# Kernel optimization log

Hardware: AMD Instinct MI355X
Metric: run time of the kernel (lower is better)

The kernel has to match this reference:

```python
import jax, jax.numpy as jnp
import numpy as np

MAX_SEQ = 4096
HEADS = 4
LOCAL_HEADS = 1
WINDOW = 128
B, N, D_IN, D, D_OUT = 8, 3000, 128, 512, 64


def setup_inputs():
    key = jax.random.key(0)
    ks = jax.random.split(key, 9)
    s = 0.02
    return {
        'x': jax.random.normal(ks[0], (B, N, D_IN), jnp.float32),
        'W1': jax.random.normal(ks[1], (D_IN, D), jnp.float32) * s,
        'b1': jnp.zeros((D,), jnp.float32),
        'ln1_g': jnp.ones((D,), jnp.float32),
        'ln1_b': jnp.zeros((D,), jnp.float32),
        'Wq': jax.random.normal(ks[2], (D, D), jnp.float32) * s,
        'Wk': jax.random.normal(ks[3], (D, D), jnp.float32) * s,
        'Wv': jax.random.normal(ks[4], (D, D), jnp.float32) * s,
        'Wo': jax.random.normal(ks[5], (D, D), jnp.float32) * s,
        'bo': jnp.zeros((D,), jnp.float32),
        'ln2_g': jnp.ones((D,), jnp.float32),
        'ln2_b': jnp.zeros((D,), jnp.float32),
        'Wf1': jax.random.normal(ks[6], (D, 4 * D), jnp.float32) * s,
        'bf1': jnp.zeros((4 * D,), jnp.float32),
        'Wf2': jax.random.normal(ks[7], (4 * D, D), jnp.float32) * s,
        'bf2': jnp.zeros((D,), jnp.float32),
        'W2': jax.random.normal(ks[8], (D, D_OUT), jnp.float32) * s,
        'b2': jnp.zeros((D_OUT,), jnp.float32),
    }


def _ln(x, g, b, eps=1e-5):
    mu = jnp.mean(x, -1, keepdims=True)
    var = jnp.var(x, -1, keepdims=True)
    return (x - mu) * jax.lax.rsqrt(var + eps) * g + b


def _look_around(x, pad_value=0.0):
    # x: [b, w, n, ...] -> [b, w, 3n, ...] (backward=1, self, forward=1 windows)
    pads = [(0, 0), (1, 1)] + [(0, 0)] * (x.ndim - 2)
    p = jnp.pad(x, pads, constant_values=pad_value)
    w = x.shape[1]
    return jnp.concatenate([p[:, i:i + w] for i in range(3)], axis=2)


def _local_attn(q, k, v):
    # windowed softmax attention, window=128, look back/forward 1 window
    Bh, H, T, d = q.shape
    w = T // WINDOW
    merge = lambda t: t.reshape(Bh * H, w, WINDOW, d)
    bq, bk, bv = merge(q), merge(k), merge(v)
    bk = _look_around(bk)
    bv = _look_around(bv)
    ticker = jnp.arange(T).reshape(1, w, WINDOW)
    bq_k = _look_around(ticker, pad_value=-1)  # [1, w, 3*WINDOW]
    dots = jnp.einsum('bwie,bwje->bwij', bq, bk) * (d ** -0.5)
    mask = (bq_k[:, :, None, :] == -1)
    dots = jnp.where(mask, jnp.finfo(dots.dtype).min, dots)
    attn = jax.nn.softmax(dots, axis=-1)
    out = jnp.einsum('bwij,bwje->bwie', attn, bv)
    return out.reshape(Bh, H, T, d)


def _linear_attn(q, k, v):
    # kernelized global attention: softmax feature maps + d x d context
    d = q.shape[-1]
    q = jax.nn.softmax(q, axis=-1) * (d ** -0.5)
    k = jax.nn.softmax(k, axis=-2)
    ctx = jnp.einsum('bhnd,bhne->bhde', k, v)
    return jnp.einsum('bhnd,bhde->bhne', q, ctx)


def _self_attn(x, Wq, Wk, Wv, Wo, bo):
    Bx, T, Dm = x.shape
    dh = Dm // HEADS
    split = lambda t: t.reshape(Bx, T, HEADS, dh).transpose(0, 2, 1, 3)
    q, k, v = split(x @ Wq), split(x @ Wk), split(x @ Wv)
    lq, gq = q[:, :LOCAL_HEADS], q[:, LOCAL_HEADS:]
    lk, gk = k[:, :LOCAL_HEADS], k[:, LOCAL_HEADS:]
    lv, gv = v[:, :LOCAL_HEADS], v[:, LOCAL_HEADS:]
    local_out = _local_attn(lq, lk, lv)
    global_out = _linear_attn(gq, gk, gv)
    out = jnp.concatenate([local_out, global_out], axis=1)
    out = out.transpose(0, 2, 1, 3).reshape(Bx, T, Dm)
    return out @ Wo + bo


def _forward(x, W1, b1, ln1_g, ln1_b, Wq, Wk, Wv, Wo, bo,
             ln2_g, ln2_b, Wf1, bf1, Wf2, bf2, W2, b2):
    Bx, n, _ = x.shape
    xp = jnp.pad(x, ((0, 0), (0, MAX_SEQ - n), (0, 0)))
    h = jnp.tanh(xp @ W1 + b1)
    # depth=1 transformer block: PreNorm attn + residual, PreNorm FF + residual
    h = h + _self_attn(_ln(h, ln1_g, ln1_b), Wq, Wk, Wv, Wo, bo)
    ff = jax.nn.gelu(_ln(h, ln2_g, ln2_b) @ Wf1 + bf1, approximate=False)
    h = h + ff @ Wf2 + bf2
    out = h @ W2 + b2
    return out[:, :n, :]


def reference(x, W1, b1, ln1_g, ln1_b, Wq, Wk, Wv, Wo, bo,
              ln2_g, ln2_b, Wf1, bf1, Wf2, bf2, W2, b2):
    return _forward(x, W1, b1, ln1_g, ln1_b, Wq, Wk, Wv, Wo, bo,
                    ln2_g, ln2_b, Wf1, bf1, Wf2, bf2, W2, b2)
```

## Files before the change

### kernel.cpp

```cpp
#include <hip/hip_runtime.h>
#include <hip/hip_bf16.h>
#include <math.h>


typedef __hip_bfloat16 bf16;
typedef __attribute__((ext_vector_type(8))) short short8;
typedef __attribute__((ext_vector_type(4))) float floatx4;

#define SEQ   4096
#define NBAT  8
#define DM    512
#define DINP  128
#define DFF   2048
#define NREAL 3000
#define CS    40

#define MFMA16(a,b,c) __builtin_amdgcn_mfma_f32_16x16x32_bf16((a),(b),(c),0,0,0)
#define BARRIER() asm volatile("s_barrier" ::: "memory")

__device__ __forceinline__ void gload_lds16(const void* g, void* l) {
  auto* gp = reinterpret_cast<const __attribute__((address_space(1))) unsigned int*>(
      reinterpret_cast<uintptr_t>(g));
  auto* lp = reinterpret_cast<__attribute__((address_space(3))) unsigned int*>(
      reinterpret_cast<uintptr_t>(l));
  __builtin_amdgcn_global_load_lds(gp, lp, 16, 0, 0);
}

__device__ __forceinline__ short8 lds_read128(const bf16* p) {
  auto* lp = reinterpret_cast<const __attribute__((address_space(3))) bf16*>(
      reinterpret_cast<uintptr_t>(p));
  short8 r;
  asm volatile("ds_read_b128 %0, %1" : "=v"(r) : "v"(lp));
  return r;
}

__device__ __forceinline__ float fast_erff(float x) {
  float ax = fabsf(x);
  float t = __builtin_amdgcn_rcpf(fmaf(0.3275911f, ax, 1.f));
  float p = fmaf(fmaf(fmaf(fmaf(1.061405429f, t, -1.453152027f), t,
                           1.421413741f), t, -0.284496736f), t, 0.254829592f) * t;
  float r = 1.f - p * __expf(-ax * ax);
  return copysignf(r, x);
}

__device__ __forceinline__ float fast_tanhf(float x) {
  float e = __expf(2.f * x);
  return 1.f - 2.f * __builtin_amdgcn_rcpf(e + 1.f);
}

__global__ __launch_bounds__(256) void beacon(float* __restrict__ out, long n) {
  long i = (long)blockIdx.x * 256 + threadIdx.x;
  if (i < n) out[i] = 10000.f;
}

__global__ __launch_bounds__(256) void transpose8(
    const float* __restrict__ W1, const float* __restrict__ Wq,
    const float* __restrict__ Wk, const float* __restrict__ Wv,
    const float* __restrict__ Wo, const float* __restrict__ Wf1,
    const float* __restrict__ Wf2, const float* __restrict__ W2,
    bf16* __restrict__ wt) {
  const int Ks[8]   = {128, 512, 512, 512, 512, 512, 2048, 512};
  const int Ns[8]   = {512, 512, 512, 512, 512, 2048, 512, 64};
  const int Nps[8]  = {512, 512, 512, 512, 512, 2048, 512, 128};
  const long Ofs[8] = {0L, 65536L, 327680L, 589824L, 851968L, 1114112L, 2162688L, 3211264L};
  int zi = blockIdx.z;
  int K = Ks[zi], N = Ns[zi], Npad = Nps[zi];
  int k0 = blockIdx.x * 64, n0 = blockIdx.y * 64;
  if (k0 >= K || n0 >= Npad) return;
  const float* W = zi == 0 ? W1 : zi == 1 ? Wq : zi == 2 ? Wk : zi == 3 ? Wv
                 : zi == 4 ? Wo : zi == 5 ? Wf1 : zi == 6 ? Wf2 : W2;
  bf16* Wt = wt + Ofs[zi];
  __shared__ float t[64][65];
  int r = threadIdx.x >> 2, c = (threadIdx.x & 3) * 16;
#pragma unroll
  for (int i = 0; i < 16; i++) {
    int n = n0 + c + i;
    t[r][c + i] = (n < N) ? W[(long)(k0 + r) * N + n] : 0.f;
  }
  __syncthreads();
#pragma unroll
  for (int i = 0; i < 16; i++)
    Wt[(long)(n0 + r) * K + k0 + c + i] = (bf16)t[c + i][r];
}

__device__ inline uint4 pack8(const float* p) {
  union { bf16 h[8]; uint4 u; } r;
  float4 a = *(const float4*)p;
  float4 b = *(const float4*)(p + 4);
  r.h[0] = (bf16)a.x; r.h[1] = (bf16)a.y; r.h[2] = (bf16)a.z; r.h[3] = (bf16)a.w;
  r.h[4] = (bf16)b.x; r.h[5] = (bf16)b.y; r.h[6] = (bf16)b.z; r.h[7] = (bf16)b.w;
  return r.u;
}

__global__ __launch_bounds__(512, 2) void gemm256(
    const bf16* __restrict__ A, const bf16* __restrict__ Bt,
    const float* __restrict__ bias, float* __restrict__ Cf, bf16* __restrict__ Cb,
    int K, int lda, int ldb, int ldc, int EPI,
    long aBatch, long bBatch, int zdiv, long cOuter, long cInner) {
  __shared__ __align__(16) bf16 sm[2][2][256 * 64];
  const int tid = threadIdx.x;
  const int lane = tid & 63, wid = tid >> 6;

  const int nx = gridDim.x, ny = gridDim.y;
  const long nwg = (long)nx * ny * gridDim.z;
  const long fid = blockIdx.x + (long)nx * (blockIdx.y + (long)ny * blockIdx.z);
  const long cq = nwg >> 3, cr = nwg & 7;
  const long xcd = fid & 7, ofs = fid >> 3;
  const long swz = (xcd < cr ? xcd * (cq + 1) : cr * (cq + 1) + (xcd - cr) * cq) + ofs;
  const int bx = (int)(swz % nx);
  const int by = (int)((swz / nx) % ny);
  const int bz = (int)(swz / ((long)nx * ny));

  const bf16* Ab = A + (long)bz * aBatch;
  const bf16* Bb = Bt + (long)bz * bBatch;
  const long cOff = (long)(bz / zdiv) * cOuter + (long)(bz % zdiv) * cInner;
  const int row0 = by * 256;
  const int col0 = bx * 256;

  const int widm = wid >> 2, widn = wid & 3;
  const int lr = lane & 15, lq4 = lane >> 4;
  const int sw = (lr & 7) << 4;
  const int k0e = ((0 * 64 + lq4 * 16) ^ sw) >> 1;
  const int k1e = ((1 * 64 + lq4 * 16) ^ sw) >> 1;

  const int lrow = lane >> 3;
  const int lch = (lane & 7) ^ lrow;
  const bf16* pAbase = Ab + (long)(row0 + wid * 8 + lrow) * lda + lch * 8;
  const bf16* pBbase = Bb + (long)(col0 + wid * 8 + lrow) * ldb + lch * 8;
  const long a64 = (long)64 * lda, b64 = (long)64 * ldb;
  int kA = 0, kB = 0;

  floatx4 acc[8][4];
#pragma unroll
  for (int i = 0; i < 8; i++)
#pragma unroll
    for (int j = 0; j < 4; j++) acc[i][j] = {0.f, 0.f, 0.f, 0.f};

  auto stageA = [&](int buf, int h) {
    bf16* d = &sm[buf][0][(h * 128 + wid * 8) * 64];
    const bf16* g = pAbase + (long)(h * 2) * a64 + kA;
    gload_lds16(g, d);
    gload_lds16(g + a64, d + 64 * 64);
  };
  auto stageB = [&](int buf, int h) {
    bf16* d = &sm[buf][1][(h * 128 + wid * 8) * 64];
    const bf16* g = pBbase + (long)(h * 2) * b64 + kB;
    gload_lds16(g, d);
    gload_lds16(g + b64, d + 64 * 64);
  };

  short8 bfr[4][2], af[2][2];
  auto readB = [&](int buf) {
    const bf16* base = &sm[buf][1][0];
#pragma unroll
    for (int nt = 0; nt < 4; nt++) {
      int colB = widn * 64 + nt * 16 + lr;
      bfr[nt][0] = lds_read128(base + colB * 64 + k0e);
      bfr[nt][1] = lds_read128(base + colB * 64 + k1e);
    }
  };
  auto readA = [&](int buf, int q) {
    const bf16* base = &sm[buf][0][0];
#pragma unroll
    for (int m = 0; m < 2; m++) {
      int rowA = widm * 128 + q * 32 + m * 16 + lr;
      af[m][0] = lds_read128(base + rowA * 64 + k0e);
      af[m][1] = lds_read128(base + rowA * 64 + k1e);
    }
  };
  auto mmaq = [&](int q) {
    asm volatile("s_waitcnt lgkmcnt(0)" ::: "memory");
    __builtin_amdgcn_sched_barrier(0);
    __builtin_amdgcn_s_setprio(1);
#pragma unroll
    for (int m = 0; m < 2; m++)
#pragma unroll
      for (int nt = 0; nt < 4; nt++) {
        acc[q * 2 + m][nt] = MFMA16(af[m][0], bfr[nt][0], acc[q * 2 + m][nt]);
        acc[q * 2 + m][nt] = MFMA16(af[m][1], bfr[nt][1], acc[q * 2 + m][nt]);
      }
    __builtin_amdgcn_s_setprio(0);
  };

  const int T = K >> 6;
  stageA(0, 0); stageA(0, 1); kA += 64;
  stageB(0, 0); stageB(0, 1); kB += 64;
  stageB(1, 0); stageB(1, 1); kB += 64;
  asm volatile("s_waitcnt vmcnt(4)" ::: "memory");
  BARRIER();

  for (int t = 0; t < T; t++) {
    const int cb = t & 1, nb = cb ^ 1;
    readB(cb);
    readA(cb, 0);
    if (t + 1 < T) stageA(nb, 0);
    mmaq(0);
    BARRIER();
    readA(cb, 1);
    if (t + 1 < T) { stageA(nb, 1); kA += 64; }
    if (t + 2 < T) stageB(cb, 0);
    mmaq(1);
    BARRIER();
    readA(cb, 2);
    if (t + 2 < T) { stageB(cb, 1); kB += 64; }
    mmaq(2);
    BARRIER();
    readA(cb, 3);
    mmaq(3);
    if (t + 2 < T) {
      asm volatile("s_waitcnt vmcnt(4)" ::: "memory");
    } else if (t + 1 < T) {
      asm volatile("s_waitcnt vmcnt(0)" ::: "memory");
    }
    BARRIER();
  }

  if (EPI == 2) {
#pragma unroll
    for (int nt = 0; nt < 4; nt++) {
      int c = col0 + widn * 64 + nt * 16 + lr;
      float bv = bias ? bias[c] : 0.f;
#pragma unroll
      for (int mi = 0; mi < 8; mi++) {
        long rb = row0 + widm * 128 + mi * 16 + lq4 * 4;
#pragma unroll
        for (int reg = 0; reg < 4; reg++) {
          float v = acc[mi][nt][reg] + bv;
          long idx = cOff + (rb + reg) * (long)ldc + c;
          Cf[idx] += v;
        }
      }
    }
  } else {
    bf16* scr = ((bf16*)&sm[0][0][0]) + wid * (64 * 80);
    const int rr = lane >> 3, ccol = (lane & 7) * 8;
#pragma unroll
    for (int p = 0; p < 2; p++) {
#pragma unroll
      for (int nt = 0; nt < 4; nt++) {
        int c = col0 + widn * 64 + nt * 16 + lr;
        float bv = bias ? bias[c] : 0.f;
#pragma unroll
        for (int ml = 0; ml < 4; ml++) {
#pragma unroll
          for (int reg = 0; reg < 4; reg++) {
            float v = acc[p * 4 + ml][nt][reg] + bv;
            if (EPI == 4) v = 0.5f * v * (1.f + fast_erff(v * 0.70710678118654752f));
            scr[(ml * 16 + lq4 * 4 + reg) * 80 + nt * 16 + lr] = (bf16)v;
          }
        }
      }
#pragma unroll
      for (int it = 0; it < 8; it++) {
        int r = it * 8 + rr;
        uint4 v = *(const uint4*)&scr[r * 80 + ccol];
        long grow = row0 + widm * 128 + p * 64 + r;
        *(uint4*)&Cb[cOff + grow * (long)ldc + col0 + widn * 64 + ccol] = v;
      }
    }
  }
}

__global__ __launch_bounds__(256) void gemm_bt(
    const void* __restrict__ Avoid, const bf16* __restrict__ Bt,
    const float* __restrict__ bias, float* __restrict__ Cf, bf16* __restrict__ Cb,
    int K, int lda, int ldb, int ldc, int EPI, int AMODE,
    long aBatch, long bBatch, int zdiv, long cOuter, long cInner) {
  __shared__ __align__(16) bf16 As0[128 * 32];
  __shared__ __align__(16) bf16 As1[128 * 32];
  __shared__ __align__(16) bf16 Bs0[128 * 32];
  __shared__ __align__(16) bf16 Bs1[128 * 32];
  const int tid = threadIdx.x;

  const int nx = gridDim.x, ny = gridDim.y;
  const long nwg = (long)nx * ny * gridDim.z;
  const long fid = blockIdx.x + (long)nx * (blockIdx.y + (long)ny * blockIdx.z);
  const long cq = nwg >> 3, cr = nwg & 7;
  const long xcd = fid & 7, ofs = fid >> 3;
  const long swz = (xcd < cr ? xcd * (cq + 1) : cr * (cq + 1) + (xcd - cr) * cq) + ofs;
  const int bx = (int)(swz % nx);
  const int by = (int)((swz / nx) % ny);
  const int bz = (int)(swz / ((long)nx * ny));

  Bt += (long)bz * bBatch;
  const long cOff = (long)(bz / zdiv) * cOuter + (long)(bz % zdiv) * cInner;
  const int row0 = by * 128;
  const int col0 = bx * 128;
  const int lane = tid & 63, wid = tid >> 6;
  const int wm = (wid & 1) * 64, wn = (wid >> 1) * 64;
  const int lr = lane & 15, lk = (lane >> 4) * 8;

  floatx4 acc[4][4];
#pragma unroll
  for (int i = 0; i < 4; i++)
#pragma unroll
    for (int j = 0; j < 4; j++) acc[i][j] = {0.f, 0.f, 0.f, 0.f};

  if (AMODE == 0) {
    const bf16* A = (const bf16*)Avoid + (long)bz * aBatch;
    const bf16* pAa = A + (long)(row0 + wid * 16 + (lane >> 2)) * lda + (lane & 3) * 8;
    const bf16* pBa = Bt + (long)(col0 + wid * 16 + (lane >> 2)) * ldb + (lane & 3) * 8;
    bf16* ldsA0 = &As0[wid * 16 * 32];
    bf16* ldsA1 = &As1[wid * 16 * 32];
    bf16* ldsB0 = &Bs0[wid * 16 * 32];
    bf16* ldsB1 = &Bs1[wid * 16 * 32];
    const long a64 = (long)64 * lda, b64 = (long)64 * ldb;

    auto stage = [&](bf16* dA, bf16* dB) {
      gload_lds16(pAa, dA);
      gload_lds16(pAa + a64, dA + 64 * 32);
      gload_lds16(pBa, dB);
      gload_lds16(pBa + b64, dB + 64 * 32);
      pAa += 32; pBa += 32;
    };
    auto compute = [&](const bf16* AS, const bf16* BS) {
      short8 af[4], bfr[4];
#pragma unroll
      for (int mt = 0; mt < 4; mt++) af[mt] = *(const short8*)(&AS[(wm + mt * 16 + lr) * 32 + lk]);
#pragma unroll
      for (int nt = 0; nt < 4; nt++) bfr[nt] = *(const short8*)(&BS[(wn + nt * 16 + lr) * 32 + lk]);
#pragma unroll
      for (int mt = 0; mt < 4; mt++)
#pragma unroll
        for (int nt = 0; nt < 4; nt++)
          acc[mt][nt] = MFMA16(af[mt], bfr[nt], acc[mt][nt]);
    };

    stage(ldsA0, ldsB0);
    __syncthreads();
    for (int k0 = 0; k0 < K; k0 += 64) {
      stage(ldsA1, ldsB1);
      compute(As0, Bs0);
      __syncthreads();
      if (k0 + 64 < K) stage(ldsA0, ldsB0);
      compute(As1, Bs1);
      __syncthreads();
    }
  } else {
    const float* Af = (const float*)Avoid;
    const int srow = tid >> 2;
    const int skcol = (tid & 3) * 8;
    const long r0 = row0 + srow, r1 = r0 + 64;
    const bf16* pB = Bt + (long)(col0 + srow) * ldb + skcol;
    const int ldsOff = srow * 32 + skcol;
    const float* pF0; const float* pF1;
    bool v0 = true, v1 = true;
    if (AMODE == 1) {
      int t0 = (int)(r0 & (SEQ - 1)), t1 = (int)(r1 & (SEQ - 1));
      v0 = t0 < NREAL; v1 = t1 < NREAL;
      if (!v0) t0 = 0;
      if (!v1) t1 = 0;
      pF0 = Af + ((r0 >> 12) * NREAL + t0) * DINP + skcol;
      pF1 = Af + ((r1 >> 12) * NREAL + t1) * DINP + skcol;
    } else {
      pF0 = Af + r0 * lda + skcol;
      pF1 = Af + r1 * lda + skcol;
    }
    for (int k0 = 0; k0 < K; k0 += 32) {
      uint4 b0 = *(const uint4*)(pB);
      uint4 b1 = *(const uint4*)(pB + (long)64 * ldb);
      pB += 32;
      uint4 a0 = {0, 0, 0, 0}, a1 = {0, 0, 0, 0};
      if (v0) a0 = pack8(pF0);
      if (v1) a1 = pack8(pF1);
      pF0 += 32; pF1 += 32;
      __syncthreads();
      *(uint4*)(&As0[ldsOff]) = a0;
      *(uint4*)(&As0[ldsOff + 64 * 32]) = a1;
      *(uint4*)(&Bs0[ldsOff]) = b0;
      *(uint4*)(&Bs0[ldsOff + 64 * 32]) = b1;
      __syncthreads();
      short8 af[4], bfr[4];
#pragma unroll
      for (int mt = 0; mt < 4; mt++) af[mt] = *(const short8*)(&As0[(wm + mt * 16 + lr) * 32 + lk]);
#pragma unroll
      for (int nt = 0; nt < 4; nt++) bfr[nt] = *(const short8*)(&Bs0[(wn + nt * 16 + lr) * 32 + lk]);
#pragma unroll
      for (int mt = 0; mt < 4; mt++)
#pragma unroll
        for (int nt = 0; nt < 4; nt++)
          acc[mt][nt] = MFMA16(af[mt], bfr[nt], acc[mt][nt]);
    }
  }

#pragma unroll
  for (int nt = 0; nt < 4; nt++) {
    int c = col0 + wn + nt * 16 + lr;
    float bv = 0.f;
    if (bias) {
      if (EPI == 5) { if (c < 64) bv = bias[c]; }
      else bv = bias[c];
    }
#pragma unroll
    for (int mt = 0; mt < 4; mt++) {
      long rb = row0 + wm + mt * 16 + (lane >> 4) * 4;
#pragma unroll
      for (int reg = 0; reg < 4; reg++) {
        float v = acc[mt][nt][reg] + bv;
        long ri = rb + reg;
        long idx = cOff + ri * (long)ldc + c;
        if (EPI == 0) Cf[idx] = fast_tanhf(v);
        else if (EPI == 1) Cb[idx] = (bf16)v;
        else if (EPI == 2) Cf[idx] += v;
        else if (EPI == 4) { float g = 0.5f * v * (1.f + fast_erff(v * 0.70710678118654752f)); Cb[idx] = (bf16)g; }
        else if (EPI == 5) {
          int bb = (int)(ri >> 12); int tt = (int)(ri & (SEQ - 1));
          if (tt < NREAL && c < 64) Cf[((long)bb * NREAL + tt) * 64 + c] = v;
        }
      }
    }
  }
}

__global__ __launch_bounds__(256) void ln_kernel(const float* __restrict__ h,
                                                 const float* __restrict__ g,
                                                 const float* __restrict__ bta,
                                                 bf16* __restrict__ out) {
  int wid = threadIdx.x >> 6, lane = threadIdx.x & 63;
  long row = (long)blockIdx.x * 4 + wid;
  const float* src = h + row * DM + lane * 8;
  float4 a = *(const float4*)(src);
  float4 b = *(const float4*)(src + 4);
  float x[8] = {a.x, a.y, a.z, a.w, b.x, b.y, b.z, b.w};
  float s = 0.f, sq = 0.f;
#pragma unroll
  for (int i = 0; i < 8; i++) { s += x[i]; sq += x[i] * x[i]; }
#pragma unroll
  for (int m = 32; m >= 1; m >>= 1) { s += __shfl_xor(s, m, 64); sq += __shfl_xor(sq, m, 64); }
  float mu = s * (1.f / DM);
  float var = sq * (1.f / DM) - mu * mu;
  float rstd = rsqrtf(var + 1e-5f);
  const float* gp = g + lane * 8;
  const float* bp = bta + lane * 8;
  bf16* dst = out + row * DM + lane * 8;
#pragma unroll
  for (int i = 0; i < 8; i++)
    dst[i] = (bf16)((x[i] - mu) * rstd * gp[i] + bp[i]);
}

__global__ __launch_bounds__(256) void local_attn(const bf16* __restrict__ q,
                                                  const bf16* __restrict__ k,
                                                  const bf16* __restrict__ v,
                                                  bf16* __restrict__ att) {
  int half = blockIdx.x, w = blockIdx.y, b = blockIdx.z;
  int tid = threadIdx.x, wid = tid >> 6, lane = tid & 63;
  int lr = lane & 15, lq4 = lane >> 4;
  __shared__ __align__(16) bf16 Ks[32 * 128];
  __shared__ __align__(16) bf16 Vts[128 * 32];
  __shared__ __align__(16) bf16 Ps[4][16 * 32];

  int t0 = w * 128 + half * 64 + wid * 16;
  long qbase = ((long)b * SEQ + t0 + lr) * DM;
  short8 qf[4];
#pragma unroll
  for (int ks = 0; ks < 4; ks++) qf[ks] = *(const short8*)(q + qbase + ks * 32 + lq4 * 8);

  floatx4 Oacc[8];
#pragma unroll
  for (int i = 0; i < 8; i++) Oacc[i] = {0.f, 0.f, 0.f, 0.f};
  float rs[4] = {0.f, 0.f, 0.f, 0.f};

  int keystart = w * 128 - 128;
  for (int ch = 0; ch < 12; ch++) {
    int kb = keystart + ch * 32;
    if (kb < 0 || kb >= SEQ) continue;
    {
      int j = tid >> 3, d = (tid & 7) * 16;
      const bf16* ksrc = k + ((long)b * SEQ + kb + j) * DM + d;
      *(uint4*)(&Ks[j * 128 + d]) = *(const uint4*)(ksrc);
      *(uint4*)(&Ks[j * 128 + d + 8]) = *(const uint4*)(ksrc + 8);
      const bf16* vsrc = v + ((long)b * SEQ + kb + j) * DM + d;
#pragma unroll
      for (int e = 0; e < 16; e++) Vts[(d + e) * 32 + j] = vsrc[e];
    }
    __syncthreads();
    floatx4 s0 = {0.f, 0.f, 0.f, 0.f}, s1 = {0.f, 0.f, 0.f, 0.f};
#pragma unroll
    for (int ks = 0; ks < 4; ks++) {
      short8 kf0 = *(const short8*)(&Ks[(0 + lr) * 128 + ks * 32 + lq4 * 8]);
      short8 kf1 = *(const short8*)(&Ks[(16 + lr) * 128 + ks * 32 + lq4 * 8]);
      s0 = MFMA16(qf[ks], kf0, s0);
      s1 = MFMA16(qf[ks], kf1, s1);
    }
#pragma unroll
    for (int reg = 0; reg < 4; reg++) {
      float e0 = __expf(s0[reg] * 0.08838834764831845f);
      float e1 = __expf(s1[reg] * 0.08838834764831845f);
      rs[reg] += e0 + e1;
      Ps[wid][(lq4 * 4 + reg) * 32 + lr] = (bf16)e0;
      Ps[wid][(lq4 * 4 + reg) * 32 + 16 + lr] = (bf16)e1;
    }
    __syncthreads();
    short8 pf = *(const short8*)(&Ps[wid][lr * 32 + lq4 * 8]);
#pragma unroll
    for (int nt = 0; nt < 8; nt++) {
      short8 vf = *(const short8*)(&Vts[(nt * 16 + lr) * 32 + lq4 * 8]);
      Oacc[nt] = MFMA16(pf, vf, Oacc[nt]);
    }
    __syncthreads();
  }
#pragma unroll
  for (int m = 1; m < 16; m <<= 1)
#pragma unroll
    for (int reg = 0; reg < 4; reg++) rs[reg] += __shfl_xor(rs[reg], m, 64);
  long obase = ((long)b * SEQ + t0 + lq4 * 4) * DM;
#pragma unroll
  for (int nt = 0; nt < 8; nt++)
#pragma unroll
    for (int reg = 0; reg < 4; reg++)
      att[obase + (long)reg * DM + nt * 16 + lr] = (bf16)(Oacc[nt][reg] / rs[reg]);
}

__global__ __launch_bounds__(256) void qp_softmax(const bf16* __restrict__ q, bf16* __restrict__ qp) {
  int wid = threadIdx.x >> 6, lane = threadIdx.x & 63;
  long task = (long)blockIdx.x * 4 + wid;
  int tt = (int)(task & (SEQ - 1));
  int z6 = (int)(task >> 12);
  int lb = z6 / 3, h2 = z6 % 3;
  const bf16* src = q + ((long)lb * SEQ + tt) * DM + (h2 + 1) * 128 + lane * 2;
  float x0 = (float)src[0], x1 = (float)src[1];
  float m = fmaxf(x0, x1);
#pragma unroll
  for (int s = 32; s >= 1; s >>= 1) m = fmaxf(m, __shfl_xor(m, s, 64));
  float e0 = __expf(x0 - m), e1 = __expf(x1 - m);
  float sm = e0 + e1;
#pragma unroll
  for (int s = 32; s >= 1; s >>= 1) sm += __shfl_xor(sm, s, 64);
  float inv = 0.08838834764831845f / sm;
  bf16* dst = qp + task * 128 + lane * 2;
  dst[0] = (bf16)(e0 * inv);
  dst[1] = (bf16)(e1 * inv);
}

__global__ __launch_bounds__(128) void kstats_part(const bf16* __restrict__ k,
                                                   float* __restrict__ part, int lOff) {
  int chunk = blockIdx.x, z = blockIdx.y;
  int lb = z / 3, h2 = z % 3, ch = (h2 + 1) * 128;
  int d = threadIdx.x;
  const bf16* base = k + ((long)lb * SEQ + chunk * 128) * DM + ch + d;
  float m = -1e30f;
#pragma unroll 4
  for (int t = 0; t < 128; t++) m = fmaxf(m, (float)base[(long)t * DM]);
  float l = 0.f;
#pragma unroll 4
  for (int t = 0; t < 128; t++) l += __expf((float)base[(long)t * DM] - m);
  int idx = (z * 32 + chunk) * 128 + d;
  part[idx] = m;
  part[lOff + idx] = l;
}

__global__ __launch_bounds__(128) void kstats_comb(const float* __restrict__ part,
                                                   float* __restrict__ kml, int lOff) {
  int z = blockIdx.x, d = threadIdx.x;
  float M = -1e30f;
#pragma unroll 4
  for (int c = 0; c < 32; c++) M = fmaxf(M, part[(z * 32 + c) * 128 + d]);
  float L = 0.f;
#pragma unroll 4
  for (int c = 0; c < 32; c++) {
    int i = (z * 32 + c) * 128 + d;
    L += part[lOff + i] * __expf(part[i] - M);
  }
  kml[z * 256 + d] = M;
  kml[z * 256 + 128 + d] = L;
}

__global__ __launch_bounds__(256) void ctx_mfma(const bf16* __restrict__ k,
                                                const bf16* __restrict__ v,
                                                const float* __restrict__ kml,
                                                float* __restrict__ part) {
  int chunk = blockIdx.x, z = blockIdx.y;
  int lb = z / 3, h2 = z % 3, ch = (h2 + 1) * 128;
  int tid = threadIdx.x, lane = tid & 63, wid = tid >> 6;
  const int wm = (wid & 1) * 64, wn = (wid >> 1) * 64;
  const int lr = lane & 15, lk = (lane >> 4) * 8;
  __shared__ float ml2[128];
  __shared__ __align__(16) bf16 Vt[128 * CS];
  __shared__ __align__(16) bf16 Kt[128 * CS];
  if (tid < 128)
    ml2[tid] = kml[z * 256 + tid] + logf(kml[z * 256 + 128 + tid]);

  int j = tid >> 3, d0 = (tid & 7) * 16;
  const bf16* vsrc = v + ((long)lb * SEQ + chunk * 512 + j) * DM + ch + d0;
  const bf16* ksrc = k + ((long)lb * SEQ + chunk * 512 + j) * DM + ch + d0;

  floatx4 acc[4][4];
#pragma unroll
  for (int i = 0; i < 4; i++)
#pragma unroll
    for (int jj = 0; jj < 4; jj++) acc[i][jj] = {0.f, 0.f, 0.f, 0.f};

  for (int s = 0; s < 16; s++) {
    union { bf16 h[16]; uint4 u[2]; } va, ka;
    va.u[0] = *(const uint4*)(vsrc); va.u[1] = *(const uint4*)(vsrc + 8);
    ka.u[0] = *(const uint4*)(ksrc); ka.u[1] = *(const uint4*)(ksrc + 8);
    vsrc += (long)32 * DM; ksrc += (long)32 * DM;
    __syncthreads();
#pragma unroll
    for (int e = 0; e < 16; e++) {
      Vt[(d0 + e) * CS + j] = va.h[e];
      Kt[(d0 + e) * CS + j] = (bf16)__expf((float)ka.h[e] - ml2[d0 + e]);
    }
    __syncthreads();
    short8 af[4], bfr[4];
#pragma unroll
    for (int mt = 0; mt < 4; mt++) af[mt] = *(const short8*)(&Vt[(wm + mt * 16 + lr) * CS + lk]);
#pragma unroll
    for (int nt = 0; nt < 4; nt++) bfr[nt] = *(const short8*)(&Kt[(wn + nt * 16 + lr) * CS + lk]);
#pragma unroll
    for (int mt = 0; mt < 4; mt++)
#pragma unroll
      for (int nt = 0; nt < 4; nt++)
        acc[mt][nt] = MFMA16(af[mt], bfr[nt], acc[mt][nt]);
  }

  float* dst = part + ((long)z * 8 + chunk) * 16384;
#pragma unroll
  for (int nt = 0; nt < 4; nt++) {
    int c = wn + nt * 16 + lr;
#pragma unroll
    for (int mt = 0; mt < 4; mt++) {
      int rb = wm + mt * 16 + (lane >> 4) * 4;
#pragma unroll
      for (int reg = 0; reg < 4; reg++)
        dst[(rb + reg) * 128 + c] = acc[mt][nt][reg];
    }
  }
}

__global__ __launch_bounds__(256) void ctx_reduce(const float* __restrict__ part, bf16* __restrict__ ctxT) {
  long i = (long)blockIdx.x * 256 + threadIdx.x;
  int z = (int)(i >> 14);
  int off = (int)(i & 16383);
  float s = 0.f;
#pragma unroll
  for (int c = 0; c < 8; c++) s += part[(((long)z * 8 + c) << 14) + off];
  ctxT[i] = (bf16)s;
}

extern "C" void kernel_launch(void* const* d_in, const int* in_sizes, int n_in,
                              void* d_out, int out_size, void* d_ws, size_t ws_size,
                              hipStream_t stream) {
  float* outp = (float*)d_out;

  long offH = 0;
  int GB = 0;
  long offLNG, offQ, offK, offV, offATT, offCTXP, offCTXT, offKML, offWT, need;
  for (int gb = 8; gb >= 2; gb >>= 1) {
    long sLN = (long)gb * 4194304;
    offLNG = 67108864L;
    offQ   = offLNG + sLN;
    offK   = offQ + sLN;
    offV   = offK + sLN;
    offATT = offV + sLN;
    offCTXP= offATT + sLN;
    offCTXT= offCTXP + (long)gb * 1572864;
    offKML = offCTXT + (long)gb * 98304;
    offWT  = offKML + (long)gb * 3072;
    need   = offWT + 6553600L;
    if ((size_t)need <= ws_size) { GB = gb; break; }
  }
  if (GB == 0) {
    beacon<<<(out_size + 255) / 256, 256, 0, stream>>>(outp, out_size);
    return;
  }
  const int NG = NBAT / GB;
  const long GR = (long)GB * SEQ;
  const int NZ = GB * 3;

  const float* x   = (const float*)d_in[0];
  const float* W1  = (const float*)d_in[1];
  const float* b1  = (const float*)d_in[2];
  const float* g1  = (const float*)d_in[3];
  const float* be1 = (const float*)d_in[4];
  const float* Wq  = (const float*)d_in[5];
  const float* Wk  = (const float*)d_in[6];
  const float* Wv  = (const float*)d_in[7];
  const float* Wo  = (const float*)d_in[8];
  const float* bo  = (const float*)d_in[9];
  const float* g2  = (const float*)d_in[10];
  const float* be2 = (const float*)d_in[11];
  const float* Wf1 = (const float*)d_in[12];
  const float* bf1 = (const float*)d_in[13];
  const float* Wf2 = (const float*)d_in[14];
  const float* bf2 = (const float*)d_in[15];
  const float* W2  = (const float*)d_in[16];
  const float* b2  = (const float*)d_in[17];

  char* ws = (char*)d_ws;
  float* h   = (float*)(ws + offH);
  bf16* lnG  = (bf16*)(ws + offLNG);
  bf16* qp   = (bf16*)(ws + offLNG);
  bf16* qb   = (bf16*)(ws + offQ);
  bf16* kb   = (bf16*)(ws + offK);
  bf16* vb   = (bf16*)(ws + offV);
  bf16* attb = (bf16*)(ws + offATT);
  bf16* ff1g = (bf16*)(ws + offQ);
  float* ctxp= (float*)(ws + offCTXP);
  bf16* ctxT = (bf16*)(ws + offCTXT);
  float* kml = (float*)(ws + offKML);
  bf16* wt   = (bf16*)(ws + offWT);
  bf16* wqt  = wt + 65536;
  bf16* wot  = wt + 851968;
  bf16* wf1t = wt + 1114112;
  bf16* wf2t = wt + 2162688;
  bf16* w2t  = wt + 3211264;
  const int lOff = NZ * 32 * 128;

  transpose8<<<dim3(32, 32, 8), 256, 0, stream>>>(W1, Wq, Wk, Wv, Wo, Wf1, Wf2, W2, wt);

  gemm_bt<<<dim3(4, 256, 1), 256, 0, stream>>>(x, wt, b1, h, nullptr,
      DINP, DINP, DINP, DM, 0, 1, 0, 0, 1, 0, 0);

  for (int g = 0; g < NG; g++) {
    float* hg = h + (long)g * GR * DM;
    ln_kernel<<<(int)(GR / 4), 256, 0, stream>>>(hg, g1, be1, lnG);
    gemm256<<<dim3(2, (int)(GR / 256), 3), 512, 0, stream>>>(lnG, wqt, nullptr, nullptr, qb,
        DM, DM, DM, DM, 1,
        0L, 262144L, 3, 0L, GR * DM);

    local_attn<<<dim3(2, 32, GB), 256, 0, stream>>>(qb, kb, vb, attb);

    qp_softmax<<<NZ * 1024, 256, 0, stream>>>(qb, qp);
    kstats_part<<<dim3(32, NZ), 128, 0, stream>>>(kb, ctxp, lOff);
    kstats_comb<<<NZ, 128, 0, stream>>>(ctxp, kml, lOff);
    ctx_mfma<<<dim3(8, NZ), 256, 0, stream>>>(kb, vb, kml, ctxp);
    ctx_reduce<<<NZ * 64, 256, 0, stream>>>(ctxp, ctxT);
    gemm_bt<<<dim3(1, 32, NZ), 256, 0, stream>>>(qp, ctxT, nullptr, nullptr, attb + 128,
        128, 128, 128, DM, 1, 0,
        (long)SEQ * 128, 16384L, 3, (long)SEQ * DM, 128L);

    gemm256<<<dim3(2, (int)(GR / 256), 1), 512, 0, stream>>>(attb, wot, bo, hg, nullptr,
        DM, DM, DM, DM, 2, 0, 0, 1, 0, 0);
  }

  for (int g = 0; g < NG; g++) {
    float* hg = h + (long)g * GR * DM;
    ln_kernel<<<(int)(GR / 4), 256, 0, stream>>>(hg, g2, be2, lnG);
    gemm256<<<dim3(8, (int)(GR / 256), 1), 512, 0, stream>>>(lnG, wf1t, bf1, nullptr, ff1g,
        DM, DM, DM, DFF, 4, 0, 0, 1, 0, 0);
    gemm256<<<dim3(2, (int)(GR / 256), 1), 512, 0, stream>>>(ff1g, wf2t, bf2, hg, nullptr,
        DFF, DFF, DFF, DM, 2, 0, 0, 1, 0, 0);
  }

  gemm_bt<<<dim3(1, 256, 1), 256, 0, stream>>>(h, w2t, b2, outp, nullptr,
      DM, DM, DM, 64, 5, 2, 0, 0, 1, 0, 0);
}
```

Before: 664.5 us.

## Switch gemm256 to 4-stage pipeline with K=32 tiles and new LDS swizzle

Restructures the 256x256 GEMM main loop from double-buffered K=64 tiles to a four-deep ring of K=32 tiles, keeping three loads in flight ahead of compute. The LDS swizzle is reworked for 32-wide rows, and each iteration now has two barriers instead of four. The aim is to hide global-load latency better and cut per-iteration synchronisation, at the cost of more loop iterations. The epilogue scratch stride shrinks to fit the new layout and gets an extra barrier before reusing shared memory.

```diff
diff --git a/kernel.cpp b/kernel.cpp
--- a/kernel.cpp
+++ b/kernel.cpp
@@ -97,7 +97,7 @@
     const float* __restrict__ bias, float* __restrict__ Cf, bf16* __restrict__ Cb,
     int K, int lda, int ldb, int ldc, int EPI,
     long aBatch, long bBatch, int zdiv, long cOuter, long cInner) {
-  __shared__ __align__(16) bf16 sm[2][2][256 * 64];
+  __shared__ __align__(16) bf16 sm[4][2][256 * 32];
   const int tid = threadIdx.x;
   const int lane = tid & 63, wid = tid >> 6;
 
@@ -119,15 +119,14 @@
 
   const int widm = wid >> 2, widn = wid & 3;
   const int lr = lane & 15, lq4 = lane >> 4;
-  const int sw = (lr & 7) << 4;
-  const int k0e = ((0 * 64 + lq4 * 16) ^ sw) >> 1;
-  const int k1e = ((1 * 64 + lq4 * 16) ^ sw) >> 1;
-
-  const int lrow = lane >> 3;
-  const int lch = (lane & 7) ^ lrow;
-  const bf16* pAbase = Ab + (long)(row0 + wid * 8 + lrow) * lda + lch * 8;
-  const bf16* pBbase = Bb + (long)(col0 + wid * 8 + lrow) * ldb + lch * 8;
-  const long a64 = (long)64 * lda, b64 = (long)64 * ldb;
+  const int swr = (lr & 3) ^ ((lr >> 2) & 3);
+  const int colRd = (lq4 ^ swr) * 8;
+
+  const int srow = lane >> 2;
+  const int sslot = (lane & 3) ^ ((srow & 3) ^ ((srow >> 2) & 3));
+  const bf16* pAbase = Ab + (long)(row0 + wid * 16 + srow) * lda + sslot * 8;
+  const bf16* pBbase = Bb + (long)(col0 + wid * 16 + srow) * ldb + sslot * 8;
+  const long a128 = (long)128 * lda, b128 = (long)128 * ldb;
   int kA = 0, kB = 0;
 
   floatx4 acc[8][4];
@@ -136,78 +135,65 @@
 #pragma unroll
     for (int j = 0; j < 4; j++) acc[i][j] = {0.f, 0.f, 0.f, 0.f};
 
-  auto stageA = [&](int buf, int h) {
-    bf16* d = &sm[buf][0][(h * 128 + wid * 8) * 64];
-    const bf16* g = pAbase + (long)(h * 2) * a64 + kA;
-    gload_lds16(g, d);
-    gload_lds16(g + a64, d + 64 * 64);
+  auto stageA = [&](int buf) {
+    bf16* d = &sm[buf][0][(wid * 16) * 32];
+    gload_lds16(pAbase + kA, d);
+    gload_lds16(pAbase + a128 + kA, d + 128 * 32);
+    kA += 32;
   };
-  auto stageB = [&](int buf, int h) {
-    bf16* d = &sm[buf][1][(h * 128 + wid * 8) * 64];
-    const bf16* g = pBbase + (long)(h * 2) * b64 + kB;
-    gload_lds16(g, d);
-    gload_lds16(g + b64, d + 64 * 64);
+  auto stageB = [&](int buf) {
+    bf16* d = &sm[buf][1][(wid * 16) * 32];
+    gload_lds16(pBbase + kB, d);
+    gload_lds16(pBbase + b128 + kB, d + 128 * 32);
+    kB += 32;
   };
 
-  short8 bfr[4][2], af[2][2];
+  short8 bfr[4], af[4];
   auto readB = [&](int buf) {
     const bf16* base = &sm[buf][1][0];
 #pragma unroll
-    for (int nt = 0; nt < 4; nt++) {
-      int colB = widn * 64 + nt * 16 + lr;
-      bfr[nt][0] = lds_read128(base + colB * 64 + k0e);
-      bfr[nt][1] = lds_read128(base + colB * 64 + k1e);
-    }
+    for (int nt = 0; nt < 4; nt++)
+      bfr[nt] = lds_read128(base + (widn * 64 + nt * 16 + lr) * 32 + colRd);
   };
-  auto readA = [&](int buf, int q) {
+  auto readA = [&](int buf, int h) {
     const bf16* base = &sm[buf][0][0];
 #pragma unroll
-    for (int m = 0; m < 2; m++) {
-      int rowA = widm * 128 + q * 32 + m * 16 + lr;
-      af[m][0] = lds_read128(base + rowA * 64 + k0e);
-      af[m][1] = lds_read128(base + rowA * 64 + k1e);
-    }
+    for (int m = 0; m < 4; m++)
+      af[m] = lds_read128(base + (widm * 128 + h * 64 + m * 16 + lr) * 32 + colRd);
   };
-  auto mmaq = [&](int q) {
+  auto mmaq = [&](int h) {
     asm volatile("s_waitcnt lgkmcnt(0)" ::: "memory");
     __builtin_amdgcn_sched_barrier(0);
     __builtin_amdgcn_s_setprio(1);
 #pragma unroll
-    for (int m = 0; m < 2; m++)
-#pragma unroll
-      for (int nt = 0; nt < 4; nt++) {
-        acc[q * 2 + m][nt] = MFMA16(af[m][0], bfr[nt][0], acc[q * 2 + m][nt]);
-        acc[q * 2 + m][nt] = MFMA16(af[m][1], bfr[nt][1], acc[q * 2 + m][nt]);
-      }
+    for (int m = 0; m < 4; m++)
+#pragma unroll
+      for (int nt = 0; nt < 4; nt++)
+        acc[h * 4 + m][nt] = MFMA16(af[m], bfr[nt], acc[h * 4 + m][nt]);
     __builtin_amdgcn_s_setprio(0);
   };
 
-  const int T = K >> 6;
-  stageA(0, 0); stageA(0, 1); kA += 64;
-  stageB(0, 0); stageB(0, 1); kB += 64;
-  stageB(1, 0); stageB(1, 1); kB += 64;
-  asm volatile("s_waitcnt vmcnt(4)" ::: "memory");
+  const int T = K >> 5;
+  stageA(0); stageB(0);
+  stageA(1); stageB(1);
+  stageA(2); stageB(2);
+  asm volatile("s_waitcnt vmcnt(8)" ::: "memory");
   BARRIER();
 
   for (int t = 0; t < T; t++) {
-    const int cb = t & 1, nb = cb ^ 1;
+    const int cb = t & 3, sb = (t + 3) & 3;
+    const bool st = (t + 3) < T;
     readB(cb);
     readA(cb, 0);
-    if (t + 1 < T) stageA(nb, 0);
+    if (st) stageA(sb);
     mmaq(0);
     BARRIER();
     readA(cb, 1);
-    if (t + 1 < T) { stageA(nb, 1); kA += 64; }
-    if (t + 2 < T) stageB(cb, 0);
+    if (st) stageB(sb);
     mmaq(1);
-    BARRIER();
-    readA(cb, 2);
-    if (t + 2 < T) { stageB(cb, 1); kB += 64; }
-    mmaq(2);
-    BARRIER();
-    readA(cb, 3);
-    mmaq(3);
-    if (t + 2 < T) {
+    if (st) {
+      asm volatile("s_waitcnt vmcnt(8)" ::: "memory");
+    } else if (t + 2 < T) {
       asm volatile("s_waitcnt vmcnt(4)" ::: "memory");
     } else if (t + 1 < T) {
       asm volatile("s_waitcnt vmcnt(0)" ::: "memory");
@@ -232,7 +218,8 @@
       }
     }
   } else {
-    bf16* scr = ((bf16*)&sm[0][0][0]) + wid * (64 * 80);
+    BARRIER();
+    bf16* scr = ((bf16*)&sm[0][0][0]) + wid * (64 * 72);
     const int rr = lane >> 3, ccol = (lane & 7) * 8;
 #pragma unroll
     for (int p = 0; p < 2; p++) {
@@ -246,14 +233,14 @@
           for (int reg = 0; reg < 4; reg++) {
             float v = acc[p * 4 + ml][nt][reg] + bv;
             if (EPI == 4) v = 0.5f * v * (1.f + fast_erff(v * 0.70710678118654752f));
-            scr[(ml * 16 + lq4 * 4 + reg) * 80 + nt * 16 + lr] = (bf16)v;
+            scr[(ml * 16 + lq4 * 4 + reg) * 72 + nt * 16 + lr] = (bf16)v;
           }
         }
       }
 #pragma unroll
       for (int it = 0; it < 8; it++) {
         int r = it * 8 + rr;
-        uint4 v = *(const uint4*)&scr[r * 80 + ccol];
+        uint4 v = *(const uint4*)&scr[r * 72 + ccol];
         long grow = row0 + widm * 128 + p * 64 + r;
         *(uint4*)&Cb[cOff + grow * (long)ldc + col0 + widn * 64 + ccol] = v;
       }
```

Result: slower. 685.8 us (+3.2%).
